# Performance work log

Hardware: AMD Instinct MI355X
Metric: run time of the kernel (lower is better)

Reference implementation:

```python
import jax, jax.numpy as jnp
import numpy as np

# FP4 (E2M1) code table: nibble = [sign(1) | exp(2) | mantissa(1)]
# magnitudes for codes 0..7: 0, 0.5, 1, 1.5, 2, 3, 4, 6; codes 8..15 are negated.
_MAG = np.array([0.0, 0.5, 1.0, 1.5, 2.0, 3.0, 4.0, 6.0], dtype=np.float32)
FP4_LUT = jnp.asarray(np.concatenate([_MAG, -_MAG]))  # [16]

BLOCK = 16  # scale-factor block size along in_features


def setup_inputs() -> dict:
    key = jax.random.key(0)
    k0, k1, k2, k3, k4 = jax.random.split(key, 5)
    M, K, N = 32, 8192, 8192  # tokens, in_features, out_features
    inp = jax.random.normal(k0, (M, K), dtype=jnp.float32)
    qweight = jax.random.randint(k1, (N, K // 2), 0, 256, dtype=jnp.int32)  # packed FP4 pairs
    scales = jax.random.uniform(k2, (N, K // BLOCK), dtype=jnp.float32)      # per-block scales
    amax = jax.random.uniform(k3, (1,), dtype=jnp.float32) + 0.5             # global scale
    bias = jax.random.normal(k4, (N,), dtype=jnp.float32)
    return {"input": inp, "qweight": qweight, "scales": scales, "amax": amax, "bias": bias}


def _dequantize(qweight, scales, amax):
    N = qweight.shape[0]
    low = qweight & 0xF            # first element of each pair
    high = (qweight >> 4) & 0xF    # second element
    nibbles = jnp.stack([low, high], axis=-1).reshape(N, -1)  # [N, K]
    vals = FP4_LUT[nibbles]                                   # [N, K] fp4 values
    # per-block scaling: block of BLOCK contiguous in-features shares one scale
    w = (vals.reshape(N, -1, BLOCK) * scales[..., None]).reshape(N, -1)
    return w * amax[0]


def reference(input, qweight, scales, amax, bias):
    weight = _dequantize(qweight, scales, amax)   # [N, K] full-precision weight
    return input @ weight.T + bias                # F.linear
```

## Files before the change

### kernel.cpp

```cpp
#include <hip/hip_runtime.h>
#include <hip/hip_bf16.h>

#define M_DIM 32
#define K_DIM 8192
#define N_DIM 8192
#define KS 32
#define KCH (K_DIM / KS)
#define ITERS (KCH / 32)
#define NGPB 4
#define MAIN_BLOCKS ((N_DIM / 32 / NGPB) * KS)

#define A_STRIDE (KCH + 8)
#define S_STRIDE (KCH / 16 + 1)

typedef _Float16 half8   __attribute__((ext_vector_type(8)));
typedef _Float16 half2_t __attribute__((ext_vector_type(2)));
typedef float    floatx4 __attribute__((ext_vector_type(4)));

#if defined(__has_builtin)
#if __has_builtin(__builtin_amdgcn_cvt_scalef32_pk_f16_fp4)
#define HAVE_CVT_FP4 1
#endif
#endif

#ifndef HAVE_CVT_FP4
__device__ __forceinline__ uint32_t dec2(uint32_t q) {
  uint32_t c0 = q & 0xFu, c1 = (q >> 4) & 0xFu;
  uint32_t m0 = c0 & 7u, m1 = c1 & 7u;
  uint32_t t0 = min(28u * m0, m0 + 28u);
  uint32_t t1 = min(28u * m1, m1 + 28u);
  return (t0 << 9) | ((c0 & 8u) << 12)
       | (t1 << 25) | ((c1 & 8u) << 28);
}
#endif

__device__ __forceinline__ half8 decode8(int4 q, float scale) {
  union { uint32_t u[4]; half2_t h2[4]; half8 h; } w;
#ifdef HAVE_CVT_FP4
  w.h2[0] = __builtin_amdgcn_cvt_scalef32_pk_f16_fp4((unsigned)q.x, 1.0f, 0);
  w.h2[1] = __builtin_amdgcn_cvt_scalef32_pk_f16_fp4((unsigned)q.y, 1.0f, 0);
  w.h2[2] = __builtin_amdgcn_cvt_scalef32_pk_f16_fp4((unsigned)q.z, 1.0f, 0);
  w.h2[3] = __builtin_amdgcn_cvt_scalef32_pk_f16_fp4((unsigned)q.w, 1.0f, 0);
#else
  w.u[0] = dec2((uint32_t)q.x);
  w.u[1] = dec2((uint32_t)q.y);
  w.u[2] = dec2((uint32_t)q.z);
  w.u[3] = dec2((uint32_t)q.w);
#endif
  _Float16 s = (_Float16)scale;
  half8 sv = {s, s, s, s, s, s, s, s};
  return w.h * sv;
}

__global__ void init_out_kernel(floatx4* __restrict__ out4,
                                const floatx4* __restrict__ bias4) {
  int idx = blockIdx.x * blockDim.x + threadIdx.x;
  out4[idx] = bias4[idx & (N_DIM / 4 - 1)];
}

__global__ __launch_bounds__(256, 6) void fp4_linear_kernel(
    const float* __restrict__ inp,
    const int4*  __restrict__ qw4,
    const float* __restrict__ scales,
    const float* __restrict__ amaxp,
    float* __restrict__ out)
{
  __shared__ _Float16 As[M_DIM * A_STRIDE];
  __shared__ float    Ss[NGPB * 32 * S_STRIDE];

  const int t    = threadIdx.x;
  const int lane = t & 63;
  const int w    = t >> 6;
  const int ks   = blockIdx.x & (KS - 1);
  const int gb   = blockIdx.x >> 5;
  const int n0   = gb * (NGPB * 32);
  const int kb   = ks * KCH;

  const float amax = amaxp[0];

  {
    const float* src = inp + kb;
    for (int p = 0; p < 4; ++p) {
      const int idx = p * 256 + t;
      const int m = idx >> 5, c = idx & 31;
      const floatx4* g =
          reinterpret_cast<const floatx4*>(src + (size_t)m * K_DIM + c * 8);
      floatx4 f0 = g[0], f1 = g[1];
      half8 h;
      h[0] = (_Float16)f0[0]; h[1] = (_Float16)f0[1];
      h[2] = (_Float16)f0[2]; h[3] = (_Float16)f0[3];
      h[4] = (_Float16)f1[0]; h[5] = (_Float16)f1[1];
      h[6] = (_Float16)f1[2]; h[7] = (_Float16)f1[3];
      *reinterpret_cast<half8*>(&As[m * A_STRIDE + c * 8]) = h;
    }
  }
  {
    const int r = t >> 1, part = t & 1;
    const float* g = scales + (size_t)(n0 + r) * (K_DIM / 16)
                   + ks * (KCH / 16) + part * 8;
    floatx4 f0 = ((const floatx4*)g)[0];
    floatx4 f1 = ((const floatx4*)g)[1];
    float* d = &Ss[r * S_STRIDE + part * 8];
    d[0] = f0[0] * amax; d[1] = f0[1] * amax;
    d[2] = f0[2] * amax; d[3] = f0[3] * amax;
    d[4] = f1[0] * amax; d[5] = f1[1] * amax;
    d[6] = f1[2] * amax; d[7] = f1[3] * amax;
  }
  __syncthreads();

  const int row  = lane & 15;
  const int quad = lane >> 4;
  const int nloc = w * 32;

  const int nA = n0 + nloc + row;
  const int nB = nA + 16;
  const int4* qrowA = qw4 + (size_t)nA * (K_DIM / 8);
  const int4* qrowB = qw4 + (size_t)nB * (K_DIM / 8);
  const _Float16* arow0 = &As[row * A_STRIDE];
  const _Float16* arow1 = &As[(row + 16) * A_STRIDE];
  const float* sAp = &Ss[(nloc + row) * S_STRIDE];
  const float* sBp = &Ss[(nloc + 16 + row) * S_STRIDE];

  floatx4 acc00 = {0.f, 0.f, 0.f, 0.f};
  floatx4 acc01 = {0.f, 0.f, 0.f, 0.f};
  floatx4 acc10 = {0.f, 0.f, 0.f, 0.f};
  floatx4 acc11 = {0.f, 0.f, 0.f, 0.f};

  int kq = kb + quad * 8;
  int4 qA = qrowA[kq >> 3];
  int4 qB = qrowB[kq >> 3];

#pragma unroll
  for (int it = 0; it < ITERS; ++it) {
    const int nidx = min((kq + 32) >> 3, K_DIM / 8 - 1);
    int4 qA_n = qrowA[nidx];
    int4 qB_n = qrowB[nidx];

    const int klo = it * 32 + quad * 8;
    half8 a0 = *reinterpret_cast<const half8*>(arow0 + klo);
    half8 a1 = *reinterpret_cast<const half8*>(arow1 + klo);
    const int kbl = klo >> 4;
    half8 bA = decode8(qA, sAp[kbl]);
    half8 bB = decode8(qB, sBp[kbl]);

    acc00 = __builtin_amdgcn_mfma_f32_16x16x32_f16(a0, bA, acc00, 0, 0, 0);
    acc01 = __builtin_amdgcn_mfma_f32_16x16x32_f16(a0, bB, acc01, 0, 0, 0);
    acc10 = __builtin_amdgcn_mfma_f32_16x16x32_f16(a1, bA, acc10, 0, 0, 0);
    acc11 = __builtin_amdgcn_mfma_f32_16x16x32_f16(a1, bB, acc11, 0, 0, 0);

    qA = qA_n; qB = qB_n;
    kq += 32;
  }

#pragma unroll
  for (int r = 0; r < 4; ++r) {
    const int m = quad * 4 + r;
    float* o0 = out + (size_t)m * N_DIM + n0 + nloc;
    float* o1 = out + (size_t)(m + 16) * N_DIM + n0 + nloc;
    unsafeAtomicAdd(o0 + row,      acc00[r]);
    unsafeAtomicAdd(o0 + 16 + row, acc01[r]);
    unsafeAtomicAdd(o1 + row,      acc10[r]);
    unsafeAtomicAdd(o1 + 16 + row, acc11[r]);
  }
}

extern "C" void kernel_launch(void* const* d_in, const int* in_sizes, int n_in,
                              void* d_out, int out_size, void* d_ws, size_t ws_size,
                              hipStream_t stream) {
  const float* inp    = (const float*)d_in[0];
  const int4*  qw4    = (const int4*)d_in[1];
  const float* scales = (const float*)d_in[2];
  const float* amaxp  = (const float*)d_in[3];
  const float* bias   = (const float*)d_in[4];
  float* out = (float*)d_out;

  init_out_kernel<<<M_DIM * N_DIM / 4 / 256, 256, 0, stream>>>(
      (floatx4*)out, (const floatx4*)bias);
  fp4_linear_kernel<<<MAIN_BLOCKS, 256, 0, stream>>>(
      inp, qw4, scales, amaxp, out);
}
```

Measured before the change: 236.3 us.

## Stage weights through LDS with register prefetch and reduce split-K partials

The kernel now loads quantized weights, activations and scales in 128-wide K chunks into registers, stores them to LDS, and prefetches the next chunk while computing the current one. This replaces direct per-lane global weight loads and the full-slice activation preload. The K split is halved to 16. When the workspace is large enough, each split writes its partial sums to workspace and a separate reduce kernel adds them with the bias, replacing float atomics. The trade-off is an extra partial-buffer write and read (16x32x8192 floats), one more kernel launch, and lower occupancy from the launch bound of 3.

Result: slower. 242.6 us (+2.7%).

```diff
diff --git a/kernel.cpp b/kernel.cpp
--- a/kernel.cpp
+++ b/kernel.cpp
@@ -4,16 +4,24 @@
 #define M_DIM 32
 #define K_DIM 8192
 #define N_DIM 8192
-#define KS 32
+#define KS 16
 #define KCH (K_DIM / KS)
-#define ITERS (KCH / 32)
-#define NGPB 4
-#define MAIN_BLOCKS ((N_DIM / 32 / NGPB) * KS)
-
-#define A_STRIDE (KCH + 8)
-#define S_STRIDE (KCH / 16 + 1)
+#define CHK 128
+#define NCHK (KCH / CHK)
+#define STEPS (CHK / 32)
+#define NPB 128
+#define NBLK (N_DIM / NPB)
+#define MAIN_BLOCKS (NBLK * KS)
+
+#define QW_ROW (K_DIM / 8)
+#define SC_ROW (K_DIM / 16)
+
+#define QROW 17
+#define AROW 136
+#define SROW 9
 
 typedef _Float16 half8   __attribute__((ext_vector_type(8)));
+typedef _Float16 half4_t __attribute__((ext_vector_type(4)));
 typedef _Float16 half2_t __attribute__((ext_vector_type(2)));
 typedef float    floatx4 __attribute__((ext_vector_type(4)));
 
@@ -58,109 +66,138 @@
   out4[idx] = bias4[idx & (N_DIM / 4 - 1)];
 }
 
-__global__ __launch_bounds__(256, 6) void fp4_linear_kernel(
+__global__ void reduce_kernel(const floatx4* __restrict__ part,
+                              const floatx4* __restrict__ bias4,
+                              floatx4* __restrict__ out4) {
+  int idx = blockIdx.x * blockDim.x + threadIdx.x;
+  floatx4 acc = bias4[idx & (N_DIM / 4 - 1)];
+#pragma unroll
+  for (int s = 0; s < KS; ++s)
+    acc += part[(size_t)s * (M_DIM * N_DIM / 4) + idx];
+  out4[idx] = acc;
+}
+
+template <bool PARTIAL>
+__global__ __launch_bounds__(256, 3) void fp4_linear_kernel(
     const float* __restrict__ inp,
     const int4*  __restrict__ qw4,
     const float* __restrict__ scales,
     const float* __restrict__ amaxp,
-    float* __restrict__ out)
+    float* __restrict__ outp)
 {
-  __shared__ _Float16 As[M_DIM * A_STRIDE];
-  __shared__ float    Ss[NGPB * 32 * S_STRIDE];
+  __shared__ int4     Qs[NPB * QROW];
+  __shared__ _Float16 As[M_DIM * AROW];
+  __shared__ float    Ss[NPB * SROW];
 
   const int t    = threadIdx.x;
   const int lane = t & 63;
   const int w    = t >> 6;
   const int ks   = blockIdx.x & (KS - 1);
-  const int gb   = blockIdx.x >> 5;
-  const int n0   = gb * (NGPB * 32);
+  const int nb   = blockIdx.x >> 4;
+  const int n0   = nb * NPB;
   const int kb   = ks * KCH;
-
   const float amax = amaxp[0];
 
-  {
-    const float* src = inp + kb;
+  int4    qreg[8];
+  floatx4 areg[4];
+  floatx4 sreg;
+
+  auto load_chunk = [&](int kc) {
+    const int4* qbase = qw4 + (kc >> 3);
+#pragma unroll
+    for (int p = 0; p < 8; ++p) {
+      const int r = p * 16 + (t >> 4);
+      qreg[p] = qbase[(size_t)(n0 + r) * QW_ROW + (t & 15)];
+    }
+    const float* abase = inp + kc;
+#pragma unroll
     for (int p = 0; p < 4; ++p) {
-      const int idx = p * 256 + t;
-      const int m = idx >> 5, c = idx & 31;
-      const floatx4* g =
-          reinterpret_cast<const floatx4*>(src + (size_t)m * K_DIM + c * 8);
-      floatx4 f0 = g[0], f1 = g[1];
-      half8 h;
-      h[0] = (_Float16)f0[0]; h[1] = (_Float16)f0[1];
-      h[2] = (_Float16)f0[2]; h[3] = (_Float16)f0[3];
-      h[4] = (_Float16)f1[0]; h[5] = (_Float16)f1[1];
-      h[6] = (_Float16)f1[2]; h[7] = (_Float16)f1[3];
-      *reinterpret_cast<half8*>(&As[m * A_STRIDE + c * 8]) = h;
-    }
-  }
-  {
-    const int r = t >> 1, part = t & 1;
-    const float* g = scales + (size_t)(n0 + r) * (K_DIM / 16)
-                   + ks * (KCH / 16) + part * 8;
-    floatx4 f0 = ((const floatx4*)g)[0];
-    floatx4 f1 = ((const floatx4*)g)[1];
-    float* d = &Ss[r * S_STRIDE + part * 8];
-    d[0] = f0[0] * amax; d[1] = f0[1] * amax;
-    d[2] = f0[2] * amax; d[3] = f0[3] * amax;
-    d[4] = f1[0] * amax; d[5] = f1[1] * amax;
-    d[6] = f1[2] * amax; d[7] = f1[3] * amax;
-  }
-  __syncthreads();
+      const int r = p * 8 + (t >> 5);
+      areg[p] = ((const floatx4*)(abase + (size_t)r * K_DIM))[t & 31];
+    }
+    sreg = ((const floatx4*)(scales + (size_t)(n0 + (t >> 1)) * SC_ROW
+                             + (kc >> 4)))[t & 1];
+  };
+
+  auto store_chunk = [&]() {
+#pragma unroll
+    for (int p = 0; p < 8; ++p)
+      Qs[(p * 16 + (t >> 4)) * QROW + (t & 15)] = qreg[p];
+#pragma unroll
+    for (int p = 0; p < 4; ++p) {
+      floatx4 f = areg[p];
+      half4_t h;
+      h[0] = (_Float16)f[0]; h[1] = (_Float16)f[1];
+      h[2] = (_Float16)f[2]; h[3] = (_Float16)f[3];
+      *(half4_t*)&As[(p * 8 + (t >> 5)) * AROW + (t & 31) * 4] = h;
+    }
+    float* sd = &Ss[(t >> 1) * SROW + (t & 1) * 4];
+    sd[0] = sreg[0] * amax; sd[1] = sreg[1] * amax;
+    sd[2] = sreg[2] * amax; sd[3] = sreg[3] * amax;
+  };
 
   const int row  = lane & 15;
   const int quad = lane >> 4;
   const int nloc = w * 32;
-
-  const int nA = n0 + nloc + row;
-  const int nB = nA + 16;
-  const int4* qrowA = qw4 + (size_t)nA * (K_DIM / 8);
-  const int4* qrowB = qw4 + (size_t)nB * (K_DIM / 8);
-  const _Float16* arow0 = &As[row * A_STRIDE];
-  const _Float16* arow1 = &As[(row + 16) * A_STRIDE];
-  const float* sAp = &Ss[(nloc + row) * S_STRIDE];
-  const float* sBp = &Ss[(nloc + 16 + row) * S_STRIDE];
 
   floatx4 acc00 = {0.f, 0.f, 0.f, 0.f};
   floatx4 acc01 = {0.f, 0.f, 0.f, 0.f};
   floatx4 acc10 = {0.f, 0.f, 0.f, 0.f};
   floatx4 acc11 = {0.f, 0.f, 0.f, 0.f};
 
-  int kq = kb + quad * 8;
-  int4 qA = qrowA[kq >> 3];
-  int4 qB = qrowB[kq >> 3];
-
-#pragma unroll
-  for (int it = 0; it < ITERS; ++it) {
-    const int nidx = min((kq + 32) >> 3, K_DIM / 8 - 1);
-    int4 qA_n = qrowA[nidx];
-    int4 qB_n = qrowB[nidx];
-
-    const int klo = it * 32 + quad * 8;
-    half8 a0 = *reinterpret_cast<const half8*>(arow0 + klo);
-    half8 a1 = *reinterpret_cast<const half8*>(arow1 + klo);
-    const int kbl = klo >> 4;
-    half8 bA = decode8(qA, sAp[kbl]);
-    half8 bB = decode8(qB, sBp[kbl]);
-
-    acc00 = __builtin_amdgcn_mfma_f32_16x16x32_f16(a0, bA, acc00, 0, 0, 0);
-    acc01 = __builtin_amdgcn_mfma_f32_16x16x32_f16(a0, bB, acc01, 0, 0, 0);
-    acc10 = __builtin_amdgcn_mfma_f32_16x16x32_f16(a1, bA, acc10, 0, 0, 0);
-    acc11 = __builtin_amdgcn_mfma_f32_16x16x32_f16(a1, bB, acc11, 0, 0, 0);
-
-    qA = qA_n; qB = qB_n;
-    kq += 32;
+  const int4*     qApt = &Qs[(nloc + row) * QROW];
+  const int4*     qBpt = &Qs[(nloc + 16 + row) * QROW];
+  const _Float16* a0pt = &As[row * AROW];
+  const _Float16* a1pt = &As[(row + 16) * AROW];
+  const float*    sApt = &Ss[(nloc + row) * SROW];
+  const float*    sBpt = &Ss[(nloc + 16 + row) * SROW];
+
+  load_chunk(kb);
+  for (int c = 0; c < NCHK; ++c) {
+    if (c) __syncthreads();
+    store_chunk();
+    __syncthreads();
+    if (c + 1 < NCHK) load_chunk(kb + (c + 1) * CHK);
+
+#pragma unroll
+    for (int it = 0; it < STEPS; ++it) {
+      const int qi  = it * 4 + quad;
+      const int kbl = it * 2 + (quad >> 1);
+      const int klo = it * 32 + quad * 8;
+      half8 bA = decode8(qApt[qi], sApt[kbl]);
+      half8 bB = decode8(qBpt[qi], sBpt[kbl]);
+      half8 a0 = *(const half8*)(a0pt + klo);
+      half8 a1 = *(const half8*)(a1pt + klo);
+      acc00 = __builtin_amdgcn_mfma_f32_16x16x32_f16(a0, bA, acc00, 0, 0, 0);
+      acc01 = __builtin_amdgcn_mfma_f32_16x16x32_f16(a0, bB, acc01, 0, 0, 0);
+      acc10 = __builtin_amdgcn_mfma_f32_16x16x32_f16(a1, bA, acc10, 0, 0, 0);
+      acc11 = __builtin_amdgcn_mfma_f32_16x16x32_f16(a1, bB, acc11, 0, 0, 0);
+    }
   }
 
-#pragma unroll
-  for (int r = 0; r < 4; ++r) {
-    const int m = quad * 4 + r;
-    float* o0 = out + (size_t)m * N_DIM + n0 + nloc;
-    float* o1 = out + (size_t)(m + 16) * N_DIM + n0 + nloc;
-    unsafeAtomicAdd(o0 + row,      acc00[r]);
-    unsafeAtomicAdd(o0 + 16 + row, acc01[r]);
-    unsafeAtomicAdd(o1 + row,      acc10[r]);
-    unsafeAtomicAdd(o1 + 16 + row, acc11[r]);
+  if (PARTIAL) {
+    float* pb = outp + (size_t)ks * (M_DIM * N_DIM);
+#pragma unroll
+    for (int r = 0; r < 4; ++r) {
+      const int m = quad * 4 + r;
+      float* o0 = pb + (size_t)m * N_DIM + n0 + nloc;
+      float* o1 = pb + (size_t)(m + 16) * N_DIM + n0 + nloc;
+      o0[row]      = acc00[r];
+      o0[16 + row] = acc01[r];
+      o1[row]      = acc10[r];
+      o1[16 + row] = acc11[r];
+    }
+  } else {
+#pragma unroll
+    for (int r = 0; r < 4; ++r) {
+      const int m = quad * 4 + r;
+      float* o0 = outp + (size_t)m * N_DIM + n0 + nloc;
+      float* o1 = outp + (size_t)(m + 16) * N_DIM + n0 + nloc;
+      unsafeAtomicAdd(o0 + row,      acc00[r]);
+      unsafeAtomicAdd(o0 + 16 + row, acc01[r]);
+      unsafeAtomicAdd(o1 + row,      acc10[r]);
+      unsafeAtomicAdd(o1 + 16 + row, acc11[r]);
+    }
   }
 }
 
@@ -174,8 +211,17 @@
   const float* bias   = (const float*)d_in[4];
   float* out = (float*)d_out;
 
-  init_out_kernel<<<M_DIM * N_DIM / 4 / 256, 256, 0, stream>>>(
-      (floatx4*)out, (const floatx4*)bias);
-  fp4_linear_kernel<<<MAIN_BLOCKS, 256, 0, stream>>>(
-      inp, qw4, scales, amaxp, out);
-}
+  const size_t part_bytes = (size_t)KS * M_DIM * N_DIM * sizeof(float);
+  if (ws_size >= part_bytes) {
+    float* part = (float*)d_ws;
+    fp4_linear_kernel<true><<<MAIN_BLOCKS, 256, 0, stream>>>(
+        inp, qw4, scales, amaxp, part);
+    reduce_kernel<<<M_DIM * N_DIM / 4 / 256, 256, 0, stream>>>(
+        (const floatx4*)part, (const floatx4*)bias, (floatx4*)out);
+  } else {
+    init_out_kernel<<<M_DIM * N_DIM / 4 / 256, 256, 0, stream>>>(
+        (floatx4*)out, (const floatx4*)bias);
+    fp4_linear_kernel<false><<<MAIN_BLOCKS, 256, 0, stream>>>(
+        inp, qw4, scales, amaxp, out);
+  }
+}
```
